# Kernel optimization log

Measured on AMD Instinct MI355X. Metric: run time of the kernel, lower is better.

The kernel has to match this reference:

```python
import jax, jax.numpy as jnp
import numpy as np

D_MODEL = 1024
D_FF = 4096


def _layernorm(x, gamma, beta, eps=1e-5):
    mu = jnp.mean(x, axis=-1, keepdims=True)
    var = jnp.var(x, axis=-1, keepdims=True)
    return (x - mu) * jax.lax.rsqrt(var + eps) * gamma + beta


def setup_inputs() -> dict:
    key = jax.random.key(0)
    ks = jax.random.split(key, 7)
    B, S = 4, 2048
    src = jax.random.normal(ks[0], (B, S, D_MODEL), dtype=jnp.float32)
    gamma1 = jnp.ones((D_MODEL,), jnp.float32)
    beta1 = jnp.zeros((D_MODEL,), jnp.float32)
    gamma2 = jnp.ones((D_MODEL,), jnp.float32)
    beta2 = jnp.zeros((D_MODEL,), jnp.float32)
    w1 = jax.random.normal(ks[1], (D_MODEL, D_FF), jnp.float32) * (1.0 / np.sqrt(D_MODEL))
    b1 = jnp.zeros((D_FF,), jnp.float32)
    w2 = jax.random.normal(ks[2], (D_FF, D_MODEL), jnp.float32) * (1.0 / np.sqrt(D_FF))
    b2 = jnp.zeros((D_MODEL,), jnp.float32)
    return {"src": src, "gamma1": gamma1, "beta1": beta1,
            "gamma2": gamma2, "beta2": beta2,
            "w1": w1, "b1": b1, "w2": w2, "b2": b2}


def reference(src, gamma1, beta1, gamma2, beta2, w1, b1, w2, b2):
    # Pre-LN self-attention (single head, Q=K=V=norm_x, no projections)
    norm_x = _layernorm(src, gamma1, beta1)
    dim_k = norm_x.shape[-1]
    scores = jnp.einsum('bqd,bkd->bqk', norm_x, norm_x) / jnp.sqrt(jnp.float32(dim_k))
    weights = jax.nn.softmax(scores, axis=-1)
    attn = jnp.einsum('bqk,bkd->bqd', weights, norm_x)
    x = src + attn  # dropout p=0 -> identity
    # Pre-LN FFN
    h = _layernorm(x, gamma2, beta2)
    h = jax.nn.gelu(h @ w1 + b1, approximate=False)
    h = h @ w2 + b2
    return h + x
```

## Files before the change

### kernel.cpp

```cpp
#include <hip/hip_runtime.h>
#include <hip/hip_bf16.h>
#include <math.h>

typedef __attribute__((ext_vector_type(8))) short s8vec;
typedef __attribute__((ext_vector_type(16))) float f32x16;
typedef __attribute__((ext_vector_type(4))) unsigned short us4;

__device__ __forceinline__ unsigned short f2bf(float f) {
  unsigned u = __float_as_uint(f);
  u = (u + 0x7fffu + ((u >> 16) & 1u)) >> 16;
  return (unsigned short)u;
}
__device__ __forceinline__ float bf2f(unsigned short u) {
  return __uint_as_float(((unsigned)u) << 16);
}

__device__ __forceinline__ float fast_gelu(float t) {
  float t2 = t * t;
  float u = t * (1.59576912f + 0.07135481f * t2);
  float e = __expf(-u);
  return t * __frcp_rn(1.0f + e);
}

__device__ __forceinline__ void async_ld16(const unsigned short* g, unsigned short* l) {
  __builtin_amdgcn_global_load_lds(
      (__attribute__((address_space(1))) void*)g,
      (__attribute__((address_space(3))) void*)l, 16, 0, 0);
}


#define STA(q, tk, bofs)                                                    \
  async_ld16(srcA0 + (size_t)(q) * 32 * K + ((size_t)(tk) << 6),            \
             &As[(bofs) + ldsA0 + (q) * 2048])
#define STB(j, tk, bofs)                                                    \
  async_ld16(srcB0 + (size_t)(j) * 64 * K + ((size_t)(tk) << 6),            \
             &Bs[(bofs) + ldsB0 + (j) * 4096])

#define SB0() __builtin_amdgcn_sched_barrier(0)

template <int BN, int EPI>
__global__ __launch_bounds__(512, 2) void gemm_nt8(
    const unsigned short* __restrict__ A, const unsigned short* __restrict__ B,
    float* __restrict__ outF, unsigned short* __restrict__ outB,
    const float* __restrict__ bias, const float* __restrict__ res,
    int M, int N, int K,
    long long bA, long long bB, long long bO, long long bR, float scale)
{
  static_assert(BN == 256 || BN == 128, "BN must be 256 or 128");
  constexpr int NB = BN / 64;
  constexpr int NF = BN / 128;
  constexpr int WN = BN / 4;
  constexpr int ABUF = 256 * 64;
  constexpr int BBUF = BN * 64;

  __shared__ __align__(16) unsigned short As[2 * ABUF];
  __shared__ __align__(16) unsigned short Bs[2 * BBUF];

  (void)M;
  const int tid = threadIdx.x;
  const int w = tid >> 6;
  const int l = tid & 63;

  const unsigned gx = gridDim.x, gy = gridDim.y;
  unsigned lin = blockIdx.x + gx * (blockIdx.y + gy * blockIdx.z);
  const unsigned nwg = gx * gy * gridDim.z;
  lin = (lin & 7u) * (nwg >> 3) + (lin >> 3);
  const unsigned bx = lin & (gx - 1u);
  const unsigned tmp = lin >> __builtin_ctz(gx);
  const unsigned by = tmp & (gy - 1u);
  const unsigned bz = tmp >> __builtin_ctz(gy);

  const int z = (int)bz;
  A += (size_t)z * bA;
  B += (size_t)z * bB;
  const size_t tileM = (size_t)by * 256;
  const size_t tileN = (size_t)bx * BN;

  const int sub = w & 3, half = w >> 2;
  const int rA = sub * 8 + half * 128 + (l >> 3);
  const int cA = (l & 7) ^ (rA & 7) ^ ((rA >> 3) & 3);
  const unsigned short* srcA0 = A + (tileM + rA) * (size_t)K + (cA << 3);
  const int ldsA0 = (sub * 8 + half * 128) * 64;

  const int rB = w * 8 + (l >> 3);
  const int cB = (l & 7) ^ (rB & 7) ^ ((rB >> 3) & 3);
  const unsigned short* srcB0 = B + (tileN + rB) * (size_t)K + (cB << 3);
  const int ldsB0 = (w * 8) * 64;

  const int wm = half;
  const int wn = sub;
  const int fr = l & 31;
  const int fq = l >> 5;
  const int swz = (l & 7) ^ ((l >> 3) & 3);
  int pc[4];
#pragma unroll
  for (int s = 0; s < 4; ++s) pc[s] = ((((s << 1) + fq) ^ swz) << 3);
  const int aoff = (wm * 128 + fr) * 64;
  int boff[NF];
#pragma unroll
  for (int nf = 0; nf < NF; ++nf) boff[nf] = (wn * WN + nf * 32 + fr) * 64;

  f32x16 acc[4][NF] = {};
  const int NT = K >> 6;

  STA(0, 0, 0); STA(1, 0, 0); STA(2, 0, 0); STA(3, 0, 0);
#pragma unroll
  for (int j = 0; j < NB; ++j) STB(j, 0, 0);
#pragma unroll
  for (int j = 0; j < NB; ++j) STB(j, 1, BBUF);
  STA(0, 1, ABUF); STA(1, 1, ABUF);
  if constexpr (NB == 4) asm volatile("s_waitcnt vmcnt(6)" ::: "memory");
  else                   asm volatile("s_waitcnt vmcnt(4)" ::: "memory");
  __builtin_amdgcn_s_barrier();

  auto tile = [&](int t, int bf) {
    const int aB = bf * ABUF, bBo = bf * BBUF, oaB = (bf ^ 1) * ABUF;
    const bool g1 = (t + 1 < NT), g2 = (t + 2 < NT);
    s8vec b[NF][4], aA[2][4], aC[2][4];

#pragma unroll
    for (int s = 0; s < 4; ++s) {
#pragma unroll
      for (int nf = 0; nf < NF; ++nf)
        b[nf][s] = *(const s8vec*)&Bs[bBo + boff[nf] + pc[s]];
      aA[0][s] = *(const s8vec*)&As[aB + aoff + 0 * 2048 + pc[s]];
      aA[1][s] = *(const s8vec*)&As[aB + aoff + 1 * 2048 + pc[s]];
    }
    SB0();
#pragma unroll
    for (int s = 0; s < 4; ++s) {
      aC[0][s] = *(const s8vec*)&As[aB + aoff + 2 * 2048 + pc[s]];
      aC[1][s] = *(const s8vec*)&As[aB + aoff + 3 * 2048 + pc[s]];
    }
    if (g1) { STA(2, t + 1, oaB); STA(3, t + 1, oaB); }
    SB0();
    asm volatile("s_waitcnt lgkmcnt(8)" ::: "memory");
    SB0();
    __builtin_amdgcn_s_setprio(1);
#pragma unroll
    for (int s = 0; s < 4; ++s)
#pragma unroll
      for (int i = 0; i < 2; ++i)
#pragma unroll
        for (int nf = 0; nf < NF; ++nf)
          acc[i][nf] = __builtin_amdgcn_mfma_f32_32x32x16_bf16(aA[i][s], b[nf][s], acc[i][nf], 0, 0, 0);
    SB0();
    __builtin_amdgcn_s_setprio(0);
    __builtin_amdgcn_s_barrier();

    if (g2) {
#pragma unroll
      for (int j = 0; j < NB; ++j) STB(j, t + 2, bBo);
      STA(0, t + 2, aB); STA(1, t + 2, aB);
    }
    SB0();
    asm volatile("s_waitcnt lgkmcnt(0)" ::: "memory");
    SB0();
    __builtin_amdgcn_s_setprio(1);
#pragma unroll
    for (int s = 0; s < 4; ++s)
#pragma unroll
      for (int i = 0; i < 2; ++i)
#pragma unroll
        for (int nf = 0; nf < NF; ++nf)
          acc[2 + i][nf] = __builtin_amdgcn_mfma_f32_32x32x16_bf16(aC[i][s], b[nf][s], acc[2 + i][nf], 0, 0, 0);
    SB0();
    __builtin_amdgcn_s_setprio(0);
    if (g2) {
      if constexpr (NB == 4) asm volatile("s_waitcnt vmcnt(6)" ::: "memory");
      else                   asm volatile("s_waitcnt vmcnt(4)" ::: "memory");
    } else {
      asm volatile("s_waitcnt vmcnt(0)" ::: "memory");
    }
    __builtin_amdgcn_s_barrier();
  };

  for (int t = 0; t < NT; t += 2) { tile(t, 0); tile(t + 1, 1); }

  float* oF = outF + (size_t)z * bO;
  unsigned short* oB = outB + (size_t)z * bO;
  const float* rs = res + (size_t)z * bR;

  float bcol[NF];
  if (EPI >= 2) {
#pragma unroll
    for (int nf = 0; nf < NF; ++nf) bcol[nf] = bias[tileN + wn * WN + nf * 32 + fr];
  }

#pragma unroll
  for (int mf = 0; mf < 4; ++mf) {
#pragma unroll
    for (int r = 0; r < 16; ++r) {
      const size_t row = tileM + wm * 128 + (mf << 5) + (r & 3) + ((r >> 2) << 3) + (fq << 2);
      const size_t rb = row * (size_t)N;
#pragma unroll
      for (int nf = 0; nf < NF; ++nf) {
        const size_t col = tileN + wn * WN + (nf << 5) + fr;
        const float v = acc[mf][nf][r];
        if (EPI == 0) {
          oB[rb + col] = f2bf(v * scale);
        } else if (EPI == 1) {
          oF[rb + col] = v + rs[rb + col];
        } else if (EPI == 2) {
          oB[rb + col] = f2bf(fast_gelu(v + bcol[nf]));
        } else {
          oF[rb + col] = v + bcol[nf] + rs[rb + col];
        }
      }
    }
  }
}

__global__ __launch_bounds__(256) void ln_row(
    const float* __restrict__ x, const float* __restrict__ gamma,
    const float* __restrict__ beta, unsigned short* __restrict__ out)
{
  const int row = blockIdx.x;
  const float4* xr = (const float4*)(x + (size_t)row * 1024);
  const int tid = threadIdx.x;
  float4 v = xr[tid];
  float s = v.x + v.y + v.z + v.w;
  float q = v.x * v.x + v.y * v.y + v.z * v.z + v.w * v.w;
#pragma unroll
  for (int off = 32; off > 0; off >>= 1) {
    s += __shfl_down(s, off);
    q += __shfl_down(q, off);
  }
  __shared__ float rs_[4], rq_[4];
  const int w = tid >> 6, l = tid & 63;
  if (l == 0) { rs_[w] = s; rq_[w] = q; }
  __syncthreads();
  s = rs_[0] + rs_[1] + rs_[2] + rs_[3];
  q = rq_[0] + rq_[1] + rq_[2] + rq_[3];
  const float mu = s * (1.0f / 1024.0f);
  const float var = q * (1.0f / 1024.0f) - mu * mu;
  const float rstd = rsqrtf(var + 1e-5f);
  const float4 g = ((const float4*)gamma)[tid];
  const float4 b = ((const float4*)beta)[tid];
  us4 o;
  o.x = f2bf((v.x - mu) * rstd * g.x + b.x);
  o.y = f2bf((v.y - mu) * rstd * g.y + b.y);
  o.z = f2bf((v.z - mu) * rstd * g.z + b.z);
  o.w = f2bf((v.w - mu) * rstd * g.w + b.w);
  ((us4*)(out + (size_t)row * 1024))[tid] = o;
}

__global__ __launch_bounds__(256) void softmax_row(
    const unsigned short* __restrict__ sc, unsigned short* __restrict__ pr)
{
  const int row = blockIdx.x;
  const s8vec* s8 = (const s8vec*)(sc + (size_t)row * 2048);
  const int tid = threadIdx.x;
  s8vec a = s8[tid];
  float x[8];
#pragma unroll
  for (int i = 0; i < 8; ++i) x[i] = bf2f((unsigned short)a[i]);
  float mx = x[0];
#pragma unroll
  for (int i = 1; i < 8; ++i) mx = fmaxf(mx, x[i]);
#pragma unroll
  for (int off = 32; off > 0; off >>= 1) mx = fmaxf(mx, __shfl_down(mx, off));
  __shared__ float red[4];
  const int w = tid >> 6, l = tid & 63;
  if (l == 0) red[w] = mx;
  __syncthreads();
  mx = fmaxf(fmaxf(red[0], red[1]), fmaxf(red[2], red[3]));
  __syncthreads();
  float e[8], s = 0.f;
#pragma unroll
  for (int i = 0; i < 8; ++i) { e[i] = __expf(x[i] - mx); s += e[i]; }
#pragma unroll
  for (int off = 32; off > 0; off >>= 1) s += __shfl_down(s, off);
  if (l == 0) red[w] = s;
  __syncthreads();
  s = red[0] + red[1] + red[2] + red[3];
  const float inv = 1.0f / s;
  s8vec o;
#pragma unroll
  for (int i = 0; i < 8; ++i) o[i] = (short)f2bf(e[i] * inv);
  ((s8vec*)(pr + (size_t)row * 2048))[tid] = o;
}

template <bool BF16IN>
__global__ __launch_bounds__(256) void transpose_conv(
    const void* __restrict__ in_, unsigned short* __restrict__ out,
    int R, int C, long long bIn, long long bOut)
{
  __shared__ float tile[32][33];
  const int z = blockIdx.z;
  const int tx = threadIdx.x, ty = threadIdx.y;
  const int c0 = blockIdx.x * 32, r0 = blockIdx.y * 32;
  if (BF16IN) {
    const unsigned short* in = (const unsigned short*)in_ + (size_t)z * bIn;
    for (int i = ty; i < 32; i += 8)
      tile[i][tx] = bf2f(in[(size_t)(r0 + i) * C + c0 + tx]);
  } else {
    const float* in = (const float*)in_ + (size_t)z * bIn;
    for (int i = ty; i < 32; i += 8)
      tile[i][tx] = in[(size_t)(r0 + i) * C + c0 + tx];
  }
  __syncthreads();
  unsigned short* o = out + (size_t)z * bOut;
  for (int i = ty; i < 32; i += 8)
    o[(size_t)(c0 + i) * R + r0 + tx] = f2bf(tile[tx][i]);
}

extern "C" void kernel_launch(void* const* d_in, const int* in_sizes, int n_in,
                              void* d_out, int out_size, void* d_ws, size_t ws_size,
                              hipStream_t stream)
{
  (void)in_sizes; (void)n_in; (void)out_size; (void)ws_size;
  const float* src = (const float*)d_in[0];
  const float* g1  = (const float*)d_in[1];
  const float* be1 = (const float*)d_in[2];
  const float* g2  = (const float*)d_in[3];
  const float* be2 = (const float*)d_in[4];
  const float* w1  = (const float*)d_in[5];
  const float* b1  = (const float*)d_in[6];
  const float* w2  = (const float*)d_in[7];
  const float* b2  = (const float*)d_in[8];
  float* out = (float*)d_out;

  char* ws = (char*)d_ws;
  const size_t SZ_NORMX  = (size_t)8192 * 1024 * 2;
  const size_t SZ_SCORES = (size_t)4 * 2048 * 2048 * 4;
  const size_t SZ_PROBS  = (size_t)4 * 2048 * 2048 * 2;
  const size_t SZ_X      = (size_t)8192 * 1024 * 4;
  const size_t SZ_W1T    = (size_t)1024 * 4096 * 2;

  unsigned short* normx  = (unsigned short*)(ws);
  unsigned short* normxT = (unsigned short*)(ws + SZ_NORMX);
  unsigned short* scores = (unsigned short*)(ws + 2 * SZ_NORMX);
  unsigned short* probs  = (unsigned short*)(ws + 2 * SZ_NORMX + SZ_SCORES);
  float*          xbuf   = (float*)(ws + 2 * SZ_NORMX + SZ_SCORES + SZ_PROBS);
  unsigned short* w1t    = (unsigned short*)(ws + 2 * SZ_NORMX + SZ_SCORES + SZ_PROBS + SZ_X);
  unsigned short* w2t    = (unsigned short*)(ws + 2 * SZ_NORMX + SZ_SCORES + SZ_PROBS + SZ_X + SZ_W1T);
  unsigned short* normx2 = normx;
  unsigned short* hbuf   = scores;

  const dim3 tb(32, 8);
  transpose_conv<false><<<dim3(128, 32, 1), tb, 0, stream>>>(w1, w1t, 1024, 4096, 0, 0);
  transpose_conv<false><<<dim3(32, 128, 1), tb, 0, stream>>>(w2, w2t, 4096, 1024, 0, 0);

  ln_row<<<8192, 256, 0, stream>>>(src, g1, be1, normx);
  transpose_conv<true><<<dim3(32, 64, 4), tb, 0, stream>>>(
      normx, normxT, 2048, 1024, (long long)2048 * 1024, (long long)1024 * 2048);

  gemm_nt8<256, 0><<<dim3(8, 8, 4), 512, 0, stream>>>(
      normx, normx, nullptr, scores, nullptr, nullptr,
      2048, 2048, 1024,
      (long long)2048 * 1024, (long long)2048 * 1024, (long long)2048 * 2048, 0, 0.03125f);

  softmax_row<<<8192, 256, 0, stream>>>(scores, probs);

  gemm_nt8<128, 1><<<dim3(8, 8, 4), 512, 0, stream>>>(
      probs, normxT, xbuf, nullptr, nullptr, src,
      2048, 1024, 2048,
      (long long)2048 * 2048, (long long)1024 * 2048, (long long)2048 * 1024,
      (long long)2048 * 1024, 1.0f);

  ln_row<<<8192, 256, 0, stream>>>(xbuf, g2, be2, normx2);

  gemm_nt8<256, 2><<<dim3(16, 32, 1), 512, 0, stream>>>(
      normx2, w1t, nullptr, hbuf, b1, nullptr,
      8192, 4096, 1024, 0, 0, 0, 0, 1.0f);

  gemm_nt8<128, 3><<<dim3(8, 32, 1), 512, 0, stream>>>(
      hbuf, w2t, out, nullptr, b2, xbuf,
      8192, 1024, 4096, 0, 0, 0, 0, 1.0f);
}
```

Baseline: 406.8 us.

## Rework BN=256 GEMM onto 16x16x32 MFMA with phased prefetch and vectorize transposes

The BN=256 GEMM path now uses 16x16x32 bf16 MFMA fragments with a new XOR swizzle. Its loop runs one K-tile per iteration in four phases, each interleaving global prefetch of the next tile with LDS fragment loads and MFMA, under finer vmcnt waits and barriers. The BN=128 path is specialised to keep the old 32x32 scheme. The transpose-convert kernels move to 64x64 tiles with float4/8-wide loads and 4-wide stores to cut memory transactions, at the cost of more barriers per K-tile in the GEMM.

```diff
diff --git a/kernel.cpp b/kernel.cpp
--- a/kernel.cpp
+++ b/kernel.cpp
@@ -4,7 +4,9 @@
 
 typedef __attribute__((ext_vector_type(8))) short s8vec;
 typedef __attribute__((ext_vector_type(16))) float f32x16;
+typedef __attribute__((ext_vector_type(4))) float f32x4;
 typedef __attribute__((ext_vector_type(4))) unsigned short us4;
+typedef __attribute__((ext_vector_type(8))) unsigned short us8;
 
 __device__ __forceinline__ unsigned short f2bf(float f) {
   unsigned u = __float_as_uint(f);
@@ -48,8 +50,6 @@
 {
   static_assert(BN == 256 || BN == 128, "BN must be 256 or 128");
   constexpr int NB = BN / 64;
-  constexpr int NF = BN / 128;
-  constexpr int WN = BN / 4;
   constexpr int ABUF = 256 * 64;
   constexpr int BBUF = BN * 64;
 
@@ -89,122 +89,207 @@
 
   const int wm = half;
   const int wn = sub;
-  const int fr = l & 31;
-  const int fq = l >> 5;
-  const int swz = (l & 7) ^ ((l >> 3) & 3);
-  int pc[4];
-#pragma unroll
-  for (int s = 0; s < 4; ++s) pc[s] = ((((s << 1) + fq) ^ swz) << 3);
-  const int aoff = (wm * 128 + fr) * 64;
-  int boff[NF];
-#pragma unroll
-  for (int nf = 0; nf < NF; ++nf) boff[nf] = (wn * WN + nf * 32 + fr) * 64;
-
-  f32x16 acc[4][NF] = {};
   const int NT = K >> 6;
-
-  STA(0, 0, 0); STA(1, 0, 0); STA(2, 0, 0); STA(3, 0, 0);
-#pragma unroll
-  for (int j = 0; j < NB; ++j) STB(j, 0, 0);
-#pragma unroll
-  for (int j = 0; j < NB; ++j) STB(j, 1, BBUF);
-  STA(0, 1, ABUF); STA(1, 1, ABUF);
-  if constexpr (NB == 4) asm volatile("s_waitcnt vmcnt(6)" ::: "memory");
-  else                   asm volatile("s_waitcnt vmcnt(4)" ::: "memory");
-  __builtin_amdgcn_s_barrier();
-
-  auto tile = [&](int t, int bf) {
-    const int aB = bf * ABUF, bBo = bf * BBUF, oaB = (bf ^ 1) * ABUF;
-    const bool g1 = (t + 1 < NT), g2 = (t + 2 < NT);
-    s8vec b[NF][4], aA[2][4], aC[2][4];
-
-#pragma unroll
-    for (int s = 0; s < 4; ++s) {
-#pragma unroll
-      for (int nf = 0; nf < NF; ++nf)
-        b[nf][s] = *(const s8vec*)&Bs[bBo + boff[nf] + pc[s]];
-      aA[0][s] = *(const s8vec*)&As[aB + aoff + 0 * 2048 + pc[s]];
-      aA[1][s] = *(const s8vec*)&As[aB + aoff + 1 * 2048 + pc[s]];
-    }
-    SB0();
-#pragma unroll
-    for (int s = 0; s < 4; ++s) {
-      aC[0][s] = *(const s8vec*)&As[aB + aoff + 2 * 2048 + pc[s]];
-      aC[1][s] = *(const s8vec*)&As[aB + aoff + 3 * 2048 + pc[s]];
-    }
-    if (g1) { STA(2, t + 1, oaB); STA(3, t + 1, oaB); }
-    SB0();
-    asm volatile("s_waitcnt lgkmcnt(8)" ::: "memory");
-    SB0();
-    __builtin_amdgcn_s_setprio(1);
-#pragma unroll
-    for (int s = 0; s < 4; ++s)
-#pragma unroll
-      for (int i = 0; i < 2; ++i)
-#pragma unroll
-        for (int nf = 0; nf < NF; ++nf)
-          acc[i][nf] = __builtin_amdgcn_mfma_f32_32x32x16_bf16(aA[i][s], b[nf][s], acc[i][nf], 0, 0, 0);
-    SB0();
-    __builtin_amdgcn_s_setprio(0);
-    __builtin_amdgcn_s_barrier();
-
-    if (g2) {
-#pragma unroll
-      for (int j = 0; j < NB; ++j) STB(j, t + 2, bBo);
-      STA(0, t + 2, aB); STA(1, t + 2, aB);
-    }
-    SB0();
-    asm volatile("s_waitcnt lgkmcnt(0)" ::: "memory");
-    SB0();
-    __builtin_amdgcn_s_setprio(1);
-#pragma unroll
-    for (int s = 0; s < 4; ++s)
-#pragma unroll
-      for (int i = 0; i < 2; ++i)
-#pragma unroll
-        for (int nf = 0; nf < NF; ++nf)
-          acc[2 + i][nf] = __builtin_amdgcn_mfma_f32_32x32x16_bf16(aC[i][s], b[nf][s], acc[2 + i][nf], 0, 0, 0);
-    SB0();
-    __builtin_amdgcn_s_setprio(0);
-    if (g2) {
-      if constexpr (NB == 4) asm volatile("s_waitcnt vmcnt(6)" ::: "memory");
-      else                   asm volatile("s_waitcnt vmcnt(4)" ::: "memory");
-    } else {
-      asm volatile("s_waitcnt vmcnt(0)" ::: "memory");
-    }
-    __builtin_amdgcn_s_barrier();
-  };
-
-  for (int t = 0; t < NT; t += 2) { tile(t, 0); tile(t + 1, 1); }
 
   float* oF = outF + (size_t)z * bO;
   unsigned short* oB = outB + (size_t)z * bO;
   const float* rs = res + (size_t)z * bR;
 
-  float bcol[NF];
-  if (EPI >= 2) {
-#pragma unroll
-    for (int nf = 0; nf < NF; ++nf) bcol[nf] = bias[tileN + wn * WN + nf * 32 + fr];
-  }
-
-#pragma unroll
-  for (int mf = 0; mf < 4; ++mf) {
-#pragma unroll
-    for (int r = 0; r < 16; ++r) {
-      const size_t row = tileM + wm * 128 + (mf << 5) + (r & 3) + ((r >> 2) << 3) + (fq << 2);
-      const size_t rb = row * (size_t)N;
-#pragma unroll
-      for (int nf = 0; nf < NF; ++nf) {
-        const size_t col = tileN + wn * WN + (nf << 5) + fr;
-        const float v = acc[mf][nf][r];
+  if constexpr (BN == 256) {
+    const int rowi = l & 15;
+    const int kgrp = l >> 4;
+    const int fb = (l & 7) ^ ((l >> 3) & 1);
+
+    f32x4 acc[8][4] = {};
+
+#pragma unroll
+    for (int j = 0; j < 4; ++j) STB(j, 0, 0);
+    STA(0, 0, 0); STA(1, 0, 0); STA(2, 0, 0); STA(3, 0, 0);
+    asm volatile("s_waitcnt vmcnt(3)" ::: "memory");
+    __builtin_amdgcn_s_barrier();
+
+    for (int t = 0; t < NT; ++t) {
+      const int bf = t & 1;
+      const int aB = bf * ABUF, bBo = bf * BBUF;
+      const int oA = (bf ^ 1) * ABUF, oBf = (bf ^ 1) * BBUF;
+      const bool last = (t == NT - 1);
+      s8vec bfr[4][2];
+      s8vec afr[2][2];
+
+#pragma unroll
+      for (int p = 0; p < 4; ++p) {
+        if (p == 0) {
+#pragma unroll
+          for (int nf = 0; nf < 4; ++nf) {
+            const int br = (wn * 64 + nf * 16 + rowi) * 64;
+#pragma unroll
+            for (int kk = 0; kk < 2; ++kk)
+              bfr[nf][kk] = *(const s8vec*)&Bs[bBo + br +
+                  ((((kk << 2) + kgrp) ^ fb ^ ((nf << 1) & 3)) << 3)];
+          }
+        }
+#pragma unroll
+        for (int i = 0; i < 2; ++i) {
+          const int mf = 2 * p + i;
+          const int ar = (wm * 128 + mf * 16 + rowi) * 64;
+#pragma unroll
+          for (int kk = 0; kk < 2; ++kk)
+            afr[i][kk] = *(const s8vec*)&As[aB + ar +
+                ((((kk << 2) + kgrp) ^ fb ^ ((mf << 1) & 3)) << 3)];
+        }
+        if (!last) {
+          if (p == 0)      { STB(0, t + 1, oBf); STB(1, t + 1, oBf); }
+          else if (p == 1) { STB(2, t + 1, oBf); STB(3, t + 1, oBf); }
+          else if (p == 2) { STA(0, t + 1, oA);  STA(1, t + 1, oA);  }
+          else             { STA(2, t + 1, oA);  STA(3, t + 1, oA);  }
+        }
+        if (p == 0) asm volatile("s_waitcnt lgkmcnt(8)" ::: "memory");
+        SB0();
+        __builtin_amdgcn_s_barrier();
+        asm volatile("s_waitcnt lgkmcnt(0)" ::: "memory");
+        SB0();
+        __builtin_amdgcn_s_setprio(1);
+#pragma unroll
+        for (int kk = 0; kk < 2; ++kk)
+#pragma unroll
+          for (int i = 0; i < 2; ++i)
+#pragma unroll
+            for (int nf = 0; nf < 4; ++nf)
+              acc[2 * p + i][nf] = __builtin_amdgcn_mfma_f32_16x16x32_bf16(
+                  afr[i][kk], bfr[nf][kk], acc[2 * p + i][nf], 0, 0, 0);
+        SB0();
+        __builtin_amdgcn_s_setprio(0);
+        if (!last) {
+          if (p == 0)      asm volatile("s_waitcnt vmcnt(4)" ::: "memory");
+          else if (p == 1) asm volatile("s_waitcnt vmcnt(5)" ::: "memory");
+          else if (p == 2) asm volatile("s_waitcnt vmcnt(6)" ::: "memory");
+          else             asm volatile("s_waitcnt vmcnt(3)" ::: "memory");
+        } else {
+          if (p == 0)      asm volatile("s_waitcnt vmcnt(2)" ::: "memory");
+          else if (p == 1) asm volatile("s_waitcnt vmcnt(1)" ::: "memory");
+          else             asm volatile("s_waitcnt vmcnt(0)" ::: "memory");
+        }
+        __builtin_amdgcn_s_barrier();
+      }
+    }
+
+    float bcol[4];
+    if (EPI >= 2) {
+#pragma unroll
+      for (int nf = 0; nf < 4; ++nf) bcol[nf] = bias[tileN + wn * 64 + nf * 16 + rowi];
+    }
+#pragma unroll
+    for (int mf = 0; mf < 8; ++mf) {
+#pragma unroll
+      for (int r = 0; r < 4; ++r) {
+        const size_t row = tileM + wm * 128 + mf * 16 + kgrp * 4 + r;
+        const size_t rb = row * (size_t)N;
+#pragma unroll
+        for (int nf = 0; nf < 4; ++nf) {
+          const size_t col = tileN + wn * 64 + nf * 16 + rowi;
+          const float v = acc[mf][nf][r];
+          if (EPI == 0) {
+            oB[rb + col] = f2bf(v * scale);
+          } else if (EPI == 1) {
+            oF[rb + col] = v + rs[rb + col];
+          } else if (EPI == 2) {
+            oB[rb + col] = f2bf(fast_gelu(v + bcol[nf]));
+          } else {
+            oF[rb + col] = v + bcol[nf] + rs[rb + col];
+          }
+        }
+      }
+    }
+  } else {
+    const int fr = l & 31;
+    const int fq = l >> 5;
+    const int swz = (l & 7) ^ ((l >> 3) & 3);
+    int pc[4];
+#pragma unroll
+    for (int s = 0; s < 4; ++s) pc[s] = ((((s << 1) + fq) ^ swz) << 3);
+    const int aoff = (wm * 128 + fr) * 64;
+    const int boff0 = (wn * 32 + fr) * 64;
+
+    f32x16 acc[4] = {};
+
+    STA(0, 0, 0); STA(1, 0, 0); STA(2, 0, 0); STA(3, 0, 0);
+    STB(0, 0, 0); STB(1, 0, 0);
+    STB(0, 1, BBUF); STB(1, 1, BBUF);
+    STA(0, 1, ABUF); STA(1, 1, ABUF);
+    asm volatile("s_waitcnt vmcnt(4)" ::: "memory");
+    __builtin_amdgcn_s_barrier();
+
+    auto tile = [&](int t, int bf) {
+      const int aB = bf * ABUF, bBo = bf * BBUF, oaB = (bf ^ 1) * ABUF;
+      const bool g1 = (t + 1 < NT), g2 = (t + 2 < NT);
+      s8vec b[4], aA[2][4], aC[2][4];
+
+#pragma unroll
+      for (int s = 0; s < 4; ++s) {
+        b[s]     = *(const s8vec*)&Bs[bBo + boff0 + pc[s]];
+        aA[0][s] = *(const s8vec*)&As[aB + aoff + 0 * 2048 + pc[s]];
+        aA[1][s] = *(const s8vec*)&As[aB + aoff + 1 * 2048 + pc[s]];
+      }
+      SB0();
+#pragma unroll
+      for (int s = 0; s < 4; ++s) {
+        aC[0][s] = *(const s8vec*)&As[aB + aoff + 2 * 2048 + pc[s]];
+        aC[1][s] = *(const s8vec*)&As[aB + aoff + 3 * 2048 + pc[s]];
+      }
+      if (g1) { STA(2, t + 1, oaB); STA(3, t + 1, oaB); }
+      SB0();
+      asm volatile("s_waitcnt lgkmcnt(8)" ::: "memory");
+      SB0();
+      __builtin_amdgcn_s_setprio(1);
+#pragma unroll
+      for (int s = 0; s < 4; ++s)
+#pragma unroll
+        for (int i = 0; i < 2; ++i)
+          acc[i] = __builtin_amdgcn_mfma_f32_32x32x16_bf16(aA[i][s], b[s], acc[i], 0, 0, 0);
+      SB0();
+      __builtin_amdgcn_s_setprio(0);
+      __builtin_amdgcn_s_barrier();
+
+      if (g2) {
+        STB(0, t + 2, bBo); STB(1, t + 2, bBo);
+        STA(0, t + 2, aB); STA(1, t + 2, aB);
+      }
+      SB0();
+      asm volatile("s_waitcnt lgkmcnt(0)" ::: "memory");
+      SB0();
+      __builtin_amdgcn_s_setprio(1);
+#pragma unroll
+      for (int s = 0; s < 4; ++s)
+#pragma unroll
+        for (int i = 0; i < 2; ++i)
+          acc[2 + i] = __builtin_amdgcn_mfma_f32_32x32x16_bf16(aC[i][s], b[s], acc[2 + i], 0, 0, 0);
+      SB0();
+      __builtin_amdgcn_s_setprio(0);
+      if (g2) asm volatile("s_waitcnt vmcnt(4)" ::: "memory");
+      else    asm volatile("s_waitcnt vmcnt(0)" ::: "memory");
+      __builtin_amdgcn_s_barrier();
+    };
+
+    for (int t = 0; t < NT; t += 2) { tile(t, 0); tile(t + 1, 1); }
+
+    float bc;
+    if (EPI >= 2) bc = bias[tileN + wn * 32 + fr];
+#pragma unroll
+    for (int mf = 0; mf < 4; ++mf) {
+#pragma unroll
+      for (int r = 0; r < 16; ++r) {
+        const size_t row = tileM + wm * 128 + (mf << 5) + (r & 3) + ((r >> 2) << 3) + (fq << 2);
+        const size_t rb = row * (size_t)N;
+        const size_t col = tileN + wn * 32 + fr;
+        const float v = acc[mf][r];
         if (EPI == 0) {
           oB[rb + col] = f2bf(v * scale);
         } else if (EPI == 1) {
           oF[rb + col] = v + rs[rb + col];
         } else if (EPI == 2) {
-          oB[rb + col] = f2bf(fast_gelu(v + bcol[nf]));
+          oB[rb + col] = f2bf(fast_gelu(v + bc));
         } else {
-          oF[rb + col] = v + bcol[nf] + rs[rb + col];
+          oF[rb + col] = v + bc + rs[rb + col];
         }
       }
     }
@@ -281,28 +366,60 @@
   ((s8vec*)(pr + (size_t)row * 2048))[tid] = o;
 }
 
-template <bool BF16IN>
-__global__ __launch_bounds__(256) void transpose_conv(
-    const void* __restrict__ in_, unsigned short* __restrict__ out,
+__global__ __launch_bounds__(256) void tconv_f32(
+    const float* __restrict__ in, unsigned short* __restrict__ out, int R, int C)
+{
+  __shared__ float tile[64][65];
+  const int tid = threadIdx.x;
+  const int c0 = blockIdx.x * 64, r0 = blockIdx.y * 64;
+#pragma unroll
+  for (int k2 = 0; k2 < 4; ++k2) {
+    const int idx = tid + k2 * 256;
+    const int row = idx >> 4, c4 = (idx & 15) << 2;
+    const float4 v = *(const float4*)&in[(size_t)(r0 + row) * C + c0 + c4];
+    tile[row][c4] = v.x; tile[row][c4 + 1] = v.y;
+    tile[row][c4 + 2] = v.z; tile[row][c4 + 3] = v.w;
+  }
+  __syncthreads();
+#pragma unroll
+  for (int k2 = 0; k2 < 4; ++k2) {
+    const int idx = tid + k2 * 256;
+    const int cc = idx >> 4, r4 = (idx & 15) << 2;
+    us4 o;
+#pragma unroll
+    for (int j = 0; j < 4; ++j) o[j] = f2bf(tile[r4 + j][cc]);
+    *(us4*)&out[(size_t)(c0 + cc) * R + r0 + r4] = o;
+  }
+}
+
+__global__ __launch_bounds__(256) void tconv_bf16(
+    const unsigned short* __restrict__ in, unsigned short* __restrict__ out,
     int R, int C, long long bIn, long long bOut)
 {
-  __shared__ float tile[32][33];
+  __shared__ unsigned short tile[64][66];
+  const int tid = threadIdx.x;
   const int z = blockIdx.z;
-  const int tx = threadIdx.x, ty = threadIdx.y;
-  const int c0 = blockIdx.x * 32, r0 = blockIdx.y * 32;
-  if (BF16IN) {
-    const unsigned short* in = (const unsigned short*)in_ + (size_t)z * bIn;
-    for (int i = ty; i < 32; i += 8)
-      tile[i][tx] = bf2f(in[(size_t)(r0 + i) * C + c0 + tx]);
-  } else {
-    const float* in = (const float*)in_ + (size_t)z * bIn;
-    for (int i = ty; i < 32; i += 8)
-      tile[i][tx] = in[(size_t)(r0 + i) * C + c0 + tx];
-  }
-  __syncthreads();
-  unsigned short* o = out + (size_t)z * bOut;
-  for (int i = ty; i < 32; i += 8)
-    o[(size_t)(c0 + i) * R + r0 + tx] = f2bf(tile[tx][i]);
+  in += (size_t)z * bIn;
+  out += (size_t)z * bOut;
+  const int c0 = blockIdx.x * 64, r0 = blockIdx.y * 64;
+#pragma unroll
+  for (int k2 = 0; k2 < 2; ++k2) {
+    const int idx = tid + k2 * 256;
+    const int row = idx >> 3, c8 = (idx & 7) << 3;
+    const us8 v = *(const us8*)&in[(size_t)(r0 + row) * C + c0 + c8];
+#pragma unroll
+    for (int j = 0; j < 8; ++j) tile[row][c8 + j] = v[j];
+  }
+  __syncthreads();
+#pragma unroll
+  for (int k2 = 0; k2 < 4; ++k2) {
+    const int idx = tid + k2 * 256;
+    const int cc = idx >> 4, r4 = (idx & 15) << 2;
+    us4 o;
+#pragma unroll
+    for (int j = 0; j < 4; ++j) o[j] = tile[r4 + j][cc];
+    *(us4*)&out[(size_t)(c0 + cc) * R + r0 + r4] = o;
+  }
 }
 
 extern "C" void kernel_launch(void* const* d_in, const int* in_sizes, int n_in,
@@ -338,12 +455,11 @@
   unsigned short* normx2 = normx;
   unsigned short* hbuf   = scores;
 
-  const dim3 tb(32, 8);
-  transpose_conv<false><<<dim3(128, 32, 1), tb, 0, stream>>>(w1, w1t, 1024, 4096, 0, 0);
-  transpose_conv<false><<<dim3(32, 128, 1), tb, 0, stream>>>(w2, w2t, 4096, 1024, 0, 0);
+  tconv_f32<<<dim3(64, 16), 256, 0, stream>>>(w1, w1t, 1024, 4096);
+  tconv_f32<<<dim3(16, 64), 256, 0, stream>>>(w2, w2t, 4096, 1024);
 
   ln_row<<<8192, 256, 0, stream>>>(src, g1, be1, normx);
-  transpose_conv<true><<<dim3(32, 64, 4), tb, 0, stream>>>(
+  tconv_bf16<<<dim3(16, 32, 4), 256, 0, stream>>>(
       normx, normxT, 2048, 1024, (long long)2048 * 1024, (long long)1024 * 2048);
 
   gemm_nt8<256, 0><<<dim3(8, 8, 4), 512, 0, stream>>>(
```

After: 390.7 us. 4.0% less time.
